# Performance work log

Hardware: AMD Instinct MI355X
Metric: run time of the kernel (lower is better)

## Reference

```python
import jax, jax.numpy as jnp
import numpy as np

L2_NORM_CLIP = 1.0
NOISE_MUL = 0.1


def setup_inputs() -> dict:
    key = jax.random.key(0)
    ks = jax.random.split(key, 6)
    B, S, D, K = 8, 4096, 1024, 1024
    scale = 1.0 / np.sqrt(D)
    return {
        "q": jax.random.normal(ks[0], (B, 1, D), dtype=jnp.float32),
        "k": jax.random.normal(ks[1], (B, S, D), dtype=jnp.float32),
        "v": jax.random.normal(ks[2], (B, S, D), dtype=jnp.float32),
        "wq_w": jax.random.normal(ks[3], (D, K), dtype=jnp.float32) * scale,
        "wq_b": jnp.zeros((K,), dtype=jnp.float32),
        "wk_w": jax.random.normal(ks[4], (D, K), dtype=jnp.float32) * scale,
        "wk_b": jnp.zeros((K,), dtype=jnp.float32),
        "wv_w": jax.random.normal(ks[5], (D, K), dtype=jnp.float32) * scale,
        "wv_b": jnp.zeros((K,), dtype=jnp.float32),
    }


def reference(q, k, v, wq_w, wq_b, wk_w, wk_b, wv_w, wv_b):
    # Dense projections: [B,1,K], [B,S,K], [B,S,K]
    fq = q @ wq_w + wq_b
    fk = k @ wk_w + wk_b
    fv = v @ wv_w + wv_b

    # Sigmoid attention: [B,1,S]
    dk = jnp.asarray(fk.shape[-1], dtype=fq.dtype)
    logits = jnp.einsum("bqk,bsk->bqs", fq, fk) / jnp.sqrt(dk)
    attention_weights = jax.nn.sigmoid(logits)

    # Per-token L2 clip of values over feature axis
    v_norm = jnp.linalg.norm(fv, ord=2, axis=2, keepdims=True) / L2_NORM_CLIP
    fv_clipped = fv / jnp.maximum(1.0, v_norm)

    # Weight values and reduce over sequence: [B,1,K]
    fv_w = fv_clipped * jnp.transpose(attention_weights, (0, 2, 1))  # [B,S,K]
    seed = jnp.sum(fv_w, axis=1, keepdims=True)

    # Gaussian noise injection (fixed key for determinism)
    noise_key = jax.random.key(1234)
    noise = jax.random.normal(noise_key, seed.shape, dtype=seed.dtype)
    seed = seed + noise * (NOISE_MUL * L2_NORM_CLIP)
    return (seed, attention_weights)
```

## Files before the change

kernel.cpp:

```cpp
#include <hip/hip_runtime.h>
#include <stdint.h>


#define Bn 8
#define Sn 4096
#define Dn 1024
#define Kn 1024

typedef unsigned short u16;
typedef __attribute__((ext_vector_type(8))) unsigned short u16x8;
typedef __attribute__((ext_vector_type(8))) __bf16 bf16x8;
typedef __attribute__((ext_vector_type(4))) float f32x4;
typedef __attribute__((ext_vector_type(4))) float f32x4v;

__device__ __forceinline__ u16 f2bf(float f) {
  uint32_t x = __float_as_uint(f);
  x += 0x7FFFu + ((x >> 16) & 1u);
  return (u16)(x >> 16);
}

__device__ __forceinline__ uint32_t rotl32(uint32_t x, int d) {
  return (x << d) | (x >> (32 - d));
}
__device__ void threefry2x32(uint32_t k0, uint32_t k1, uint32_t x0, uint32_t x1,
                             uint32_t* o0, uint32_t* o1) {
  uint32_t ks0 = k0, ks1 = k1, ks2 = k0 ^ k1 ^ 0x1BD11BDAu;
  x0 += ks0; x1 += ks1;
#define TF_R4(a,b,c,d) \
  x0 += x1; x1 = rotl32(x1,a); x1 ^= x0; \
  x0 += x1; x1 = rotl32(x1,b); x1 ^= x0; \
  x0 += x1; x1 = rotl32(x1,c); x1 ^= x0; \
  x0 += x1; x1 = rotl32(x1,d); x1 ^= x0;
  TF_R4(13,15,26,6);  x0 += ks1; x1 += ks2 + 1u;
  TF_R4(17,29,16,24); x0 += ks2; x1 += ks0 + 2u;
  TF_R4(13,15,26,6);  x0 += ks0; x1 += ks1 + 3u;
  TF_R4(17,29,16,24); x0 += ks1; x1 += ks2 + 4u;
  TF_R4(13,15,26,6);  x0 += ks2; x1 += ks0 + 5u;
#undef TF_R4
  *o0 = x0; *o1 = x1;
}

__device__ float erfinv_f(float x) {
  float w = -log1pf(-x * x);
  float p;
  if (w < 5.0f) {
    w -= 2.5f;
    p = 2.81022636e-08f;
    p = fmaf(p, w, 3.43273939e-07f);
    p = fmaf(p, w, -3.5233877e-06f);
    p = fmaf(p, w, -4.39150654e-06f);
    p = fmaf(p, w, 0.00021858087f);
    p = fmaf(p, w, -0.00125372503f);
    p = fmaf(p, w, -0.00417768164f);
    p = fmaf(p, w, 0.246640727f);
    p = fmaf(p, w, 1.50140941f);
  } else {
    w = sqrtf(w) - 3.0f;
    p = -0.000200214257f;
    p = fmaf(p, w, 0.000100950558f);
    p = fmaf(p, w, 0.00134934322f);
    p = fmaf(p, w, -0.00367342844f);
    p = fmaf(p, w, 0.00573950773f);
    p = fmaf(p, w, -0.0076224613f);
    p = fmaf(p, w, 0.00943887047f);
    p = fmaf(p, w, 1.00167406f);
    p = fmaf(p, w, 2.83297682f);
  }
  return p * x;
}

__global__ void k_prep(const float* __restrict__ q, const float* __restrict__ wq,
                       const float* __restrict__ bq, float* __restrict__ fq,
                       const float* __restrict__ wv, u16* __restrict__ wvtp) {
  __shared__ u16 tile[64][72];
  int tid = threadIdx.x;
  if (blockIdx.x < 256) {
    int blk = blockIdx.x;
    int b = blk >> 5, jc = (blk >> 3) & 3, dc = blk & 7;
    int j = jc * 256 + tid;
    const float* qb = q + b * Dn;
    float acc = 0.f;
    int d0 = dc * 128;
    for (int d = d0; d < d0 + 128; ++d)
      acc = fmaf(qb[d], wq[(size_t)d * Kn + j], acc);
    if (dc == 0) acc += bq[j];
    atomicAdd(&fq[b * Kn + j], acc);
  } else {
    int idx = blockIdx.x - 256;
    int k0 = (idx & 15) * 64, n0 = (idx >> 4) * 64;
    int r = tid >> 2, c0 = (tid & 3) * 16;
#pragma unroll
    for (int i = 0; i < 4; ++i) {
      float4 vv = *reinterpret_cast<const float4*>(wv + (size_t)(k0 + r) * Kn + n0 + c0 + i * 4);
      tile[r][c0 + i * 4 + 0] = f2bf(vv.x);
      tile[r][c0 + i * 4 + 1] = f2bf(vv.y);
      tile[r][c0 + i * 4 + 2] = f2bf(vv.z);
      tile[r][c0 + i * 4 + 3] = f2bf(vv.w);
    }
    __syncthreads();
    int n_l = tid >> 2, kcl = (tid & 3) * 16;
    int n_g = n0 + n_l;
    alignas(16) u16 o[16];
#pragma unroll
    for (int i = 0; i < 16; ++i) o[i] = tile[kcl + i][n_l];
    int b0 = k0 + kcl;
    int b1 = b0 + 8;
    size_t off0 = ((size_t)(n_g >> 4) * 32 + (b0 >> 5)) * 512 +
                  (size_t)((((b0 >> 3) & 3) * 16) + (n_g & 15)) * 8;
    size_t off1 = ((size_t)(n_g >> 4) * 32 + (b1 >> 5)) * 512 +
                  (size_t)((((b1 >> 3) & 3) * 16) + (n_g & 15)) * 8;
    *reinterpret_cast<u16x8*>(wvtp + off0) = *reinterpret_cast<u16x8*>(&o[0]);
    *reinterpret_cast<u16x8*>(wvtp + off1) = *reinterpret_cast<u16x8*>(&o[8]);
  }
}

__global__ void k_gcb(const float* __restrict__ wk, const float* __restrict__ fq,
                      const float* __restrict__ bk, float* __restrict__ g,
                      float* __restrict__ cb) {
  int tid = threadIdx.x;
  if (blockIdx.x < 2048) {
    int wid = (blockIdx.x * 256 + tid) >> 6;
    int lane = tid & 63;
    int b = wid >> 10, d = wid & 1023;
    const float* row = wk + (size_t)d * Kn;
    const float* f = fq + b * Kn;
    float acc = 0.f;
    for (int j = lane; j < Kn; j += 64) acc = fmaf(row[j], f[j], acc);
    for (int m = 32; m; m >>= 1) acc += __shfl_xor(acc, m, 64);
    if (lane == 0) g[b * Dn + d] = acc;
  } else if (tid < 64) {
    int b = blockIdx.x - 2048;
    float acc = 0.f;
    for (int j = tid; j < Kn; j += 64) acc = fmaf(fq[b * Kn + j], bk[j], acc);
    for (int m = 32; m; m >>= 1) acc += __shfl_xor(acc, m, 64);
    if (tid == 0) cb[b] = acc;
  }
}

__global__ void k_attn(const float* __restrict__ kmat, const float* __restrict__ g,
                       const float* __restrict__ cb, float* __restrict__ out_attn,
                       float* __restrict__ attn_ws) {
  int row = blockIdx.x * 4 + (threadIdx.x >> 6);
  int lane = threadIdx.x & 63;
  int b = row >> 12;
  const float4* kr = reinterpret_cast<const float4*>(kmat + (size_t)row * Dn);
  const float4* gr = reinterpret_cast<const float4*>(g + b * Dn);
  float acc = 0.f;
#pragma unroll
  for (int i = 0; i < 4; ++i) {
    float4 kv = kr[lane + 64 * i];
    float4 gv = gr[lane + 64 * i];
    acc = fmaf(kv.x, gv.x, acc); acc = fmaf(kv.y, gv.y, acc);
    acc = fmaf(kv.z, gv.z, acc); acc = fmaf(kv.w, gv.w, acc);
  }
  for (int m = 32; m; m >>= 1) acc += __shfl_xor(acc, m, 64);
  if (lane == 0) {
    float logit = (acc + cb[b]) * 0.03125f;
    float s = 1.f / (1.f + expf(-logit));
    out_attn[row] = s;
    attn_ws[row] = s;
  }
}

__global__ __launch_bounds__(1024)
void k_fv(const float* __restrict__ v, const u16* __restrict__ wvtp,
          const float* __restrict__ bv, const float* __restrict__ attn,
          float* __restrict__ seed_acc) {
  __shared__ u16 As[64 * 128];
  __shared__ float nrm[64];
  __shared__ float coef[64];

  int r0 = blockIdx.x * 64;
  int b  = r0 >> 12;
  int s0 = r0 & (Sn - 1);

  int tid = threadIdx.x;
  int wave = tid >> 6, lane = tid & 63;
  int m = lane & 15, qq = lane >> 4;

  if (tid < 64) nrm[tid] = 0.f;

  f32x4 acc[4][4];
#pragma unroll
  for (int i = 0; i < 4; ++i)
#pragma unroll
    for (int j = 0; j < 4; ++j) acc[i][j] = (f32x4){0.f, 0.f, 0.f, 0.f};

  int arow = tid >> 4, achunk = tid & 15;
  const float* gA0 = v + ((size_t)(b * Sn + s0) + arow) * Dn + achunk * 8;
  int apos = (achunk ^ (arow & 15)) * 8;

  const u16* gBp = wvtp + (size_t)wave * 4 * 32 * 512 + (size_t)lane * 8;

  f32x4v pa0 = __builtin_nontemporal_load(reinterpret_cast<const f32x4v*>(gA0));
  f32x4v pa1 = __builtin_nontemporal_load(reinterpret_cast<const f32x4v*>(gA0) + 1);

  for (int k0 = 0; k0 < 1024; k0 += 128) {
    __syncthreads();
    {
      u16x8 o = { f2bf(pa0[0]), f2bf(pa0[1]), f2bf(pa0[2]), f2bf(pa0[3]),
                  f2bf(pa1[0]), f2bf(pa1[1]), f2bf(pa1[2]), f2bf(pa1[3]) };
      *reinterpret_cast<u16x8*>(&As[arow * 128 + apos]) = o;
    }
    if (k0 < 896) {
      const f32x4v* pa = reinterpret_cast<const f32x4v*>(gA0 + k0 + 128);
      pa0 = __builtin_nontemporal_load(pa);
      pa1 = __builtin_nontemporal_load(pa + 1);
    }
    __syncthreads();

#pragma unroll
    for (int j = 0; j < 4; ++j) {
      int c = j * 4 + qq;
      bf16x8 a[4];
#pragma unroll
      for (int rt = 0; rt < 4; ++rt) {
        int r = rt * 16 + m;
        u16x8 raw = *reinterpret_cast<const u16x8*>(&As[r * 128 + ((c ^ (r & 15)) * 8)]);
        a[rt] = __builtin_bit_cast(bf16x8, raw);
      }
#pragma unroll
      for (int ct = 0; ct < 4; ++ct) {
        u16x8 raw = *reinterpret_cast<const u16x8*>(
            gBp + ((size_t)ct * 32 + (k0 >> 5) + j) * 512);
        bf16x8 bb = __builtin_bit_cast(bf16x8, raw);
#pragma unroll
        for (int rt = 0; rt < 4; ++rt)
          acc[rt][ct] = __builtin_amdgcn_mfma_f32_16x16x32_bf16(a[rt], bb, acc[rt][ct], 0, 0, 0);
      }
    }
  }

  float bvv[4];
#pragma unroll
  for (int ct = 0; ct < 4; ++ct) bvv[ct] = bv[wave * 64 + ct * 16 + m];

#pragma unroll
  for (int rt = 0; rt < 4; ++rt) {
#pragma unroll
    for (int reg = 0; reg < 4; ++reg) {
      float ss = 0.f;
#pragma unroll
      for (int ct = 0; ct < 4; ++ct) {
        float f = acc[rt][ct][reg] + bvv[ct];
        ss = fmaf(f, f, ss);
      }
      ss += __shfl_xor(ss, 1, 64);
      ss += __shfl_xor(ss, 2, 64);
      ss += __shfl_xor(ss, 4, 64);
      ss += __shfl_xor(ss, 8, 64);
      if (m == 0) atomicAdd(&nrm[rt * 16 + qq * 4 + reg], ss);
    }
  }
  __syncthreads();
  if (tid < 64)
    coef[tid] = attn[b * Sn + s0 + tid] / fmaxf(1.f, sqrtf(nrm[tid]));
  __syncthreads();

#pragma unroll
  for (int ct = 0; ct < 4; ++ct) {
    float t = 0.f;
#pragma unroll
    for (int rt = 0; rt < 4; ++rt) {
#pragma unroll
      for (int reg = 0; reg < 4; ++reg) {
        float cf = coef[rt * 16 + qq * 4 + reg];
        t = fmaf(cf, acc[rt][ct][reg] + bvv[ct], t);
      }
    }
    t += __shfl_xor(t, 16, 64);
    t += __shfl_xor(t, 32, 64);
    if (qq == 0) atomicAdd(&seed_acc[b * Kn + wave * 64 + ct * 16 + m], t);
  }
}

__global__ void k_final(const float* __restrict__ seed_acc, float* __restrict__ out) {
  int t = blockIdx.x * 256 + threadIdx.x;
  uint32_t o0, o1;
  threefry2x32(0u, 1234u, 0u, (uint32_t)t, &o0, &o1);
  uint32_t bits = o0 ^ o1;
  float f = __uint_as_float((bits >> 9) | 0x3F800000u) - 1.0f;
  float lo = __uint_as_float(0xBF7FFFFFu);
  float u = f * (1.0f - lo) + lo;
  u = fmaxf(u, lo);
  out[t] = seed_acc[t] + 1.41421356237f * erfinv_f(u) * 0.1f;
}

extern "C" void kernel_launch(void* const* d_in, const int* in_sizes, int n_in,
                              void* d_out, int out_size, void* d_ws, size_t ws_size,
                              hipStream_t stream) {
  const float* q  = (const float*)d_in[0];
  const float* k  = (const float*)d_in[1];
  const float* v  = (const float*)d_in[2];
  const float* wq = (const float*)d_in[3];
  const float* bq = (const float*)d_in[4];
  const float* wk = (const float*)d_in[5];
  const float* bk = (const float*)d_in[6];
  const float* wv = (const float*)d_in[7];
  const float* bv = (const float*)d_in[8];
  float* out = (float*)d_out;
  float* ws = (float*)d_ws;

  float* fq       = ws;
  float* seed_acc = ws + 8192;
  float* g        = ws + 16384;
  float* cb       = ws + 24576;
  float* attn_ws  = ws + 24832;
  u16* wvtp = (u16*)((char*)d_ws + 262144);

  hipMemsetAsync(ws, 0, 16384 * sizeof(float), stream);
  k_prep <<<512,  256, 0, stream>>>(q, wq, bq, fq, wv, wvtp);
  k_gcb  <<<2056, 256, 0, stream>>>(wk, fq, bk, g, cb);
  k_attn <<<8192, 256, 0, stream>>>(k, g, cb, out + 8192, attn_ws);
  k_fv   <<<512, 1024, 0, stream>>>(v, wvtp, bv, attn_ws, seed_acc);
  k_final<<<32,   256, 0, stream>>>(seed_acc, out);
}
```

Before: 391.0 us.

## Double row tile in fv GEMM and register-prefetch weight fragments

The value-projection kernel now processes 128 rows per block instead of 64, with a K-step of 64, which halves the number of blocks and doubles reuse of each loaded weight fragment. Weight fragments are double-buffered in registers, so the next step's B loads are issued before the current MFMAs run. This raises per-thread accumulator and register use (8x4 accumulator tiles plus 16 prefetch vectors), which may lower occupancy or cause spills. It also leaves only 256 blocks, fewer than the 512 used before.

```diff
diff --git a/kernel.cpp b/kernel.cpp
--- a/kernel.cpp
+++ b/kernel.cpp
@@ -166,11 +166,11 @@
 void k_fv(const float* __restrict__ v, const u16* __restrict__ wvtp,
           const float* __restrict__ bv, const float* __restrict__ attn,
           float* __restrict__ seed_acc) {
-  __shared__ u16 As[64 * 128];
-  __shared__ float nrm[64];
-  __shared__ float coef[64];
-
-  int r0 = blockIdx.x * 64;
+  __shared__ u16 As[128 * 64];
+  __shared__ float nrm[128];
+  __shared__ float coef[128];
+
+  int r0 = blockIdx.x * 128;
   int b  = r0 >> 12;
   int s0 = r0 & (Sn - 1);
 
@@ -178,65 +178,83 @@
   int wave = tid >> 6, lane = tid & 63;
   int m = lane & 15, qq = lane >> 4;
 
-  if (tid < 64) nrm[tid] = 0.f;
-
-  f32x4 acc[4][4];
-#pragma unroll
-  for (int i = 0; i < 4; ++i)
+  if (tid < 128) nrm[tid] = 0.f;
+
+  f32x4 acc[8][4];
+#pragma unroll
+  for (int i = 0; i < 8; ++i)
 #pragma unroll
     for (int j = 0; j < 4; ++j) acc[i][j] = (f32x4){0.f, 0.f, 0.f, 0.f};
 
-  int arow = tid >> 4, achunk = tid & 15;
+  int arow = tid >> 3, achunk = tid & 7;
   const float* gA0 = v + ((size_t)(b * Sn + s0) + arow) * Dn + achunk * 8;
-  int apos = (achunk ^ (arow & 15)) * 8;
+  int apos = (achunk ^ (arow & 7)) * 8;
 
   const u16* gBp = wvtp + (size_t)wave * 4 * 32 * 512 + (size_t)lane * 8;
 
   f32x4v pa0 = __builtin_nontemporal_load(reinterpret_cast<const f32x4v*>(gA0));
   f32x4v pa1 = __builtin_nontemporal_load(reinterpret_cast<const f32x4v*>(gA0) + 1);
 
-  for (int k0 = 0; k0 < 1024; k0 += 128) {
-    __syncthreads();
-    {
-      u16x8 o = { f2bf(pa0[0]), f2bf(pa0[1]), f2bf(pa0[2]), f2bf(pa0[3]),
-                  f2bf(pa1[0]), f2bf(pa1[1]), f2bf(pa1[2]), f2bf(pa1[3]) };
-      *reinterpret_cast<u16x8*>(&As[arow * 128 + apos]) = o;
-    }
-    if (k0 < 896) {
-      const f32x4v* pa = reinterpret_cast<const f32x4v*>(gA0 + k0 + 128);
-      pa0 = __builtin_nontemporal_load(pa);
-      pa1 = __builtin_nontemporal_load(pa + 1);
-    }
-    __syncthreads();
-
-#pragma unroll
-    for (int j = 0; j < 4; ++j) {
-      int c = j * 4 + qq;
-      bf16x8 a[4];
-#pragma unroll
-      for (int rt = 0; rt < 4; ++rt) {
-        int r = rt * 16 + m;
-        u16x8 raw = *reinterpret_cast<const u16x8*>(&As[r * 128 + ((c ^ (r & 15)) * 8)]);
-        a[rt] = __builtin_bit_cast(bf16x8, raw);
-      }
-#pragma unroll
-      for (int ct = 0; ct < 4; ++ct) {
-        u16x8 raw = *reinterpret_cast<const u16x8*>(
-            gBp + ((size_t)ct * 32 + (k0 >> 5) + j) * 512);
-        bf16x8 bb = __builtin_bit_cast(bf16x8, raw);
-#pragma unroll
-        for (int rt = 0; rt < 4; ++rt)
-          acc[rt][ct] = __builtin_amdgcn_mfma_f32_16x16x32_bf16(a[rt], bb, acc[rt][ct], 0, 0, 0);
-      }
-    }
-  }
+  u16x8 Bc[8], Bn_[8];
+#pragma unroll
+  for (int f = 0; f < 8; ++f)
+    Bc[f] = *reinterpret_cast<const u16x8*>(
+        gBp + ((size_t)(f & 3) * 32 + (f >> 2)) * 512);
+
+#define FV_STEP(KT, BCUR, BNXT)                                               \
+  {                                                                           \
+    __syncthreads();                                                          \
+    {                                                                         \
+      u16x8 o = { f2bf(pa0[0]), f2bf(pa0[1]), f2bf(pa0[2]), f2bf(pa0[3]),     \
+                  f2bf(pa1[0]), f2bf(pa1[1]), f2bf(pa1[2]), f2bf(pa1[3]) };   \
+      *reinterpret_cast<u16x8*>(&As[arow * 64 + apos]) = o;                   \
+    }                                                                         \
+    if ((KT) < 15) {                                                          \
+      const f32x4v* pa = reinterpret_cast<const f32x4v*>(gA0 + ((KT) + 1) * 64); \
+      pa0 = __builtin_nontemporal_load(pa);                                   \
+      pa1 = __builtin_nontemporal_load(pa + 1);                               \
+    }                                                                         \
+    __syncthreads();                                                          \
+    if ((KT) < 15) {                                                          \
+      _Pragma("unroll")                                                       \
+      for (int f = 0; f < 8; ++f)                                             \
+        BNXT[f] = *reinterpret_cast<const u16x8*>(                            \
+            gBp + ((size_t)(f & 3) * 32 + ((KT) + 1) * 2 + (f >> 2)) * 512);  \
+    }                                                                         \
+    _Pragma("unroll")                                                         \
+    for (int j = 0; j < 2; ++j) {                                             \
+      int c = j * 4 + qq;                                                     \
+      bf16x8 a[8];                                                            \
+      _Pragma("unroll")                                                       \
+      for (int rt = 0; rt < 8; ++rt) {                                        \
+        int r = rt * 16 + m;                                                  \
+        u16x8 raw = *reinterpret_cast<const u16x8*>(                          \
+            &As[r * 64 + ((c ^ (r & 7)) * 8)]);                               \
+        a[rt] = __builtin_bit_cast(bf16x8, raw);                              \
+      }                                                                       \
+      _Pragma("unroll")                                                       \
+      for (int ct = 0; ct < 4; ++ct) {                                        \
+        bf16x8 bb = __builtin_bit_cast(bf16x8, BCUR[j * 4 + ct]);             \
+        _Pragma("unroll")                                                     \
+        for (int rt = 0; rt < 8; ++rt)                                        \
+          acc[rt][ct] = __builtin_amdgcn_mfma_f32_16x16x32_bf16(              \
+              a[rt], bb, acc[rt][ct], 0, 0, 0);                               \
+      }                                                                       \
+    }                                                                         \
+  }
+
+  for (int kt = 0; kt < 16; kt += 2) {
+    FV_STEP(kt, Bc, Bn_);
+    FV_STEP(kt + 1, Bn_, Bc);
+  }
+#undef FV_STEP
 
   float bvv[4];
 #pragma unroll
   for (int ct = 0; ct < 4; ++ct) bvv[ct] = bv[wave * 64 + ct * 16 + m];
 
 #pragma unroll
-  for (int rt = 0; rt < 4; ++rt) {
+  for (int rt = 0; rt < 8; ++rt) {
 #pragma unroll
     for (int reg = 0; reg < 4; ++reg) {
       float ss = 0.f;
@@ -253,7 +271,7 @@
     }
   }
   __syncthreads();
-  if (tid < 64)
+  if (tid < 128)
     coef[tid] = attn[b * Sn + s0 + tid] / fmaxf(1.f, sqrtf(nrm[tid]));
   __syncthreads();
 
@@ -261,7 +279,7 @@
   for (int ct = 0; ct < 4; ++ct) {
     float t = 0.f;
 #pragma unroll
-    for (int rt = 0; rt < 4; ++rt) {
+    for (int rt = 0; rt < 8; ++rt) {
 #pragma unroll
       for (int reg = 0; reg < 4; ++reg) {
         float cf = coef[rt * 16 + qq * 4 + reg];
@@ -312,6 +330,6 @@
   k_prep <<<512,  256, 0, stream>>>(q, wq, bq, fq, wv, wvtp);
   k_gcb  <<<2056, 256, 0, stream>>>(wk, fq, bk, g, cb);
   k_attn <<<8192, 256, 0, stream>>>(k, g, cb, out + 8192, attn_ws);
-  k_fv   <<<512, 1024, 0, stream>>>(v, wvtp, bv, attn_ws, seed_acc);
+  k_fv   <<<256, 1024, 0, stream>>>(v, wvtp, bv, attn_ws, seed_acc);
   k_final<<<32,   256, 0, stream>>>(seed_acc, out);
 }
```

Result: slower. 1.039 ms (+165.7%).
